# Optimization experiments

Hardware: AMD Instinct MI355X
Metric: run time of the kernel (lower is better)

## Reference

```python
import jax, jax.numpy as jnp
import numpy as np

POOL = 16  # in_downsampling == internal_downsampling == 16


def _conv1x1(x, w, b):
    # x: [B,C,H,W], w: [O,C], b: [O] -> [B,O,H,W]
    return jnp.einsum('oc,bchw->bohw', w, x) + b[None, :, None, None]


def _maxpool(x, k):
    return jax.lax.reduce_window(x, -jnp.inf, jax.lax.max,
                                 (1, 1, k, k), (1, 1, k, k), 'VALID')


def setup_inputs() -> dict:
    key = jax.random.key(0)
    ks = jax.random.split(key, 7)
    B, C, Ci, H, W = 4, 256, 128, 256, 256
    s_in = 1.0 / np.sqrt(C)
    return {
        'x':   jax.random.normal(ks[0], (B, C, H, W), jnp.float32),
        'f_w': jax.random.normal(ks[1], (Ci, C), jnp.float32) * s_in,
        'f_b': jax.random.normal(ks[2], (Ci,), jnp.float32) * 0.01,
        'g_w': jax.random.normal(ks[3], (Ci, C), jnp.float32) * s_in,
        'g_b': jax.random.normal(ks[4], (Ci,), jnp.float32) * 0.01,
        'h_w': jax.random.normal(ks[5], (C, C), jnp.float32) * s_in,
        'h_b': jax.random.normal(ks[6], (C,), jnp.float32) * 0.01,
    }


def reference(x, f_w, f_b, g_w, g_b, h_w, h_b):
    B, C, H, W = x.shape
    # pooled query / key features: [B, Ci, h1, w1] and [B, Ci, h2, w2]
    fv = _maxpool(_conv1x1(x, f_w, f_b), POOL)
    gv = _maxpool(_conv1x1(x, g_w, g_b), POOL)
    # dots[b,i,j,k,l] = sum_c fv[b,c,i,j] * gv[b,c,k,l]  (channel dot-product)
    dots = jnp.einsum('bcij,bckl->bijkl', fv, gv)
    Bd, h1, w1, h2, w2 = dots.shape
    # exp=True path: softmax over the flattened (h2, w2) key positions
    dots = jax.nn.softmax(dots.reshape(Bd, h1, w1, h2 * w2), axis=-1)
    dots = dots.reshape(Bd, h1, w1, h2, w2)
    # pooled values: [B, C, h2, w2]
    hv = _maxpool(_conv1x1(x, h_w, h_b), POOL)
    # weighted sum over key positions -> [B, C, h1, w1]
    out = jnp.einsum('bijkl,bckl->bcij', dots, hv)
    # bilinear upsample (align_corners=False == half-pixel, matches jax resize)
    up = jax.image.resize(out, (B, C, H, W), method='bilinear')
    return up + x
```

## Files before the change

### kernel.cpp

```cpp
#include <hip/hip_runtime.h>
#include <hip/hip_fp16.h>

typedef _Float16 f16;
typedef _Float16 f16x4_t __attribute__((ext_vector_type(4)));
typedef _Float16 f16x8_t __attribute__((ext_vector_type(8)));
typedef float    f32x4_t __attribute__((ext_vector_type(4)));

#define NB  4
#define NC  256
#define NH  256
#define NW  256

__global__ __launch_bounds__(256) void k_convert_w(
    const float* __restrict__ f_w, const float* __restrict__ g_w,
    const float* __restrict__ h_w, f16* __restrict__ wf)
{
    int id = blockIdx.x * 256 + threadIdx.x;
    int cout = id >> 8;
    float v;
    if (cout < 128)       v = f_w[id];
    else if (cout < 256)  v = g_w[id - 128*256];
    else                  v = h_w[id - 256*256];
    wf[id] = (f16)v;
}

__device__ __forceinline__ void bar_lds() {
    asm volatile("s_waitcnt lgkmcnt(0)" ::: "memory");
    __builtin_amdgcn_s_barrier();
}

__global__ __launch_bounds__(1024, 4) void k_pooled_conv(
    const float* __restrict__ x, const f16* __restrict__ wf,
    const float* __restrict__ f_b, const float* __restrict__ g_b,
    const float* __restrict__ h_b,
    float* __restrict__ pooled_fg,
    float* __restrict__ pooledT_h)
{
    __shared__ __align__(16) char smem[65536];

    const int t    = threadIdx.x;
    const int wave = t >> 6;
    const int lane = t & 63;
    const int l15  = lane & 15;
    const int lg   = lane >> 4;
    const bool isfg = (wave < 8);
    const int coutbase = isfg ? wave * 32 : 256 + (wave - 8) * 32;

    f16x8_t bfrag[2][8];
    #pragma unroll
    for (int n = 0; n < 2; n++) {
        const f16* wr = wf + (coutbase + n*16 + l15) * 256 + lg*8;
        #pragma unroll
        for (int k = 0; k < 8; k++)
            bfrag[n][k] = *(const f16x8_t*)(wr + k*32);
    }
    float biasv[2];
    #pragma unroll
    for (int n = 0; n < 2; n++) {
        int c = coutbase + n*16 + l15;
        biasv[n] = (c < 128) ? f_b[c] : (c < 256) ? g_b[c - 128] : h_b[c - 256];
    }

    const int dx  = t & 15;
    const int dyl = (t >> 4) & 1;
    const int c8  = (t >> 5) * 8;
    const unsigned page = (unsigned)(dyl*8 + (c8 >> 5));
    const unsigned slot = (unsigned)(dx | (((c8 >> 3) & 3) << 4));
    const unsigned woff = (page << 10) + slot * 16u;

    const int bid   = blockIdx.x;
    const int b     = bid >> 6;
    const int wbase = bid * 4;
    const float* xb = x + (size_t)b * (256u * 65536u);

    float vmax[2] = {-3.0e38f, -3.0e38f};

    auto loadst = [&](int gsd, float* r) {
        int win = wbase + (gsd >> 3);
        int s   = gsd & 7;
        int wi = (win >> 4) & 15, wj = win & 15;
        const float* src = xb + (size_t)c8 * 65536u
                         + (unsigned)((wi*16 + s*2 + dyl) * 256 + wj*16 + dx);
        #pragma unroll
        for (int cc = 0; cc < 8; cc++)
            r[cc] = src[(unsigned)cc * 65536u];
    };
    auto writest = [&](const float* r, int buf) {
        char* base = smem + buf * 32768;
        f16x8_t hv, lv;
        #pragma unroll
        for (int cc = 0; cc < 8; cc++) {
            float v = r[cc];
            f16 h = (f16)v;
            hv[cc] = h;
            lv[cc] = (f16)(v - (float)h);
        }
        *(f16x8_t*)(base + woff)         = hv;
        *(f16x8_t*)(base + 16384 + woff) = lv;
    };
    auto mfmast = [&](int buf) {
        const char* base = smem + buf * 32768 + lane * 16;
        #pragma unroll
        for (int m = 0; m < 2; m++) {
            f32x4_t acc0 = {0.f,0.f,0.f,0.f}, acc1 = {0.f,0.f,0.f,0.f};
            #pragma unroll
            for (int k = 0; k < 8; k++) {
                const char* p = base + ((m*8 + k) << 10);
                f16x8_t ah = *(const f16x8_t*)p;
                acc0 = __builtin_amdgcn_mfma_f32_16x16x32_f16(ah, bfrag[0][k], acc0, 0,0,0);
                acc1 = __builtin_amdgcn_mfma_f32_16x16x32_f16(ah, bfrag[1][k], acc1, 0,0,0);
                if (isfg) {
                    f16x8_t al = *(const f16x8_t*)(p + 16384);
                    acc0 = __builtin_amdgcn_mfma_f32_16x16x32_f16(al, bfrag[0][k], acc0, 0,0,0);
                    acc1 = __builtin_amdgcn_mfma_f32_16x16x32_f16(al, bfrag[1][k], acc1, 0,0,0);
                }
            }
            #pragma unroll
            for (int r = 0; r < 4; r++) {
                vmax[0] = fmaxf(vmax[0], acc0[r]);
                vmax[1] = fmaxf(vmax[1], acc1[r]);
            }
        }
    };
    auto finalize = [&](int win) {
        int wn = win & 255;
        #pragma unroll
        for (int n = 0; n < 2; n++) {
            float v = vmax[n];
            v = fmaxf(v, __shfl_xor(v, 16, 64));
            v = fmaxf(v, __shfl_xor(v, 32, 64));
            if (lane < 16) {
                float val = v + biasv[n];
                int c = coutbase + n*16 + lane;
                if (isfg) pooled_fg[((b*256 + c)  << 8) + wn] = val;
                else      pooledT_h[((b*256 + wn) << 8) + (c - 256)] = val;
            }
            vmax[n] = -3.0e38f;
        }
    };

    float rA[8], rB[8];
    loadst(0, rA);
    loadst(1, rB);
    writest(rA, 0);
    bar_lds();

    #pragma unroll 1
    for (int gs = 0; gs < 32; gs += 2) {
        if (gs + 2 < 32) loadst(gs + 2, rA);
        writest(rB, 1);
        mfmast(0);
        bar_lds();
        if (gs + 3 < 32) loadst(gs + 3, rB);
        if (gs + 2 < 32) writest(rA, 0);
        mfmast(1);
        if ((gs & 7) == 6) finalize(wbase + (gs >> 3));
        bar_lds();
    }
}

__global__ __launch_bounds__(256) void k_attn(
    const float* __restrict__ pooled_fg, const float* __restrict__ pooledT_h,
    float* __restrict__ attnout)
{
    __shared__ float red[4];
    __shared__ float p_lds[256];
    const int blk = blockIdx.x;
    const int b = blk >> 8;
    const int q = blk & 255;
    const int t = threadIdx.x;

    const float* fv = pooled_fg + ((b*256) << 8) + q;
    const float* gv = pooled_fg + ((b*256 + 128) << 8) + t;

    float s = 0.f;
    #pragma unroll 8
    for (int c = 0; c < 128; c++)
        s += fv[c << 8] * gv[c << 8];

    float m = s;
    #pragma unroll
    for (int o = 1; o < 64; o <<= 1) m = fmaxf(m, __shfl_xor(m, o, 64));
    if ((t & 63) == 0) red[t >> 6] = m;
    __syncthreads();
    m = fmaxf(fmaxf(red[0], red[1]), fmaxf(red[2], red[3]));
    __syncthreads();

    float p = expf(s - m);
    float sum = p;
    #pragma unroll
    for (int o = 1; o < 64; o <<= 1) sum += __shfl_xor(sum, o, 64);
    if ((t & 63) == 0) red[t >> 6] = sum;
    __syncthreads();
    sum = red[0] + red[1] + red[2] + red[3];
    p /= sum;
    p_lds[t] = p;
    __syncthreads();

    const float* hv = pooledT_h + (b << 16) + t;
    float acc = 0.f;
    #pragma unroll 8
    for (int k = 0; k < 256; k++)
        acc += p_lds[k] * hv[k << 8];
    attnout[((b*256 + t) << 8) + q] = acc;
}

__global__ __launch_bounds__(256) void k_upsample_add(
    const float* __restrict__ x, const float* __restrict__ attnout,
    float* __restrict__ out)
{
    __shared__ float L[256];
    const int blk = blockIdx.x;
    const int t = threadIdx.x;
    L[t] = attnout[(blk << 8) + t];
    __syncthreads();
    const float* xp = x   + (size_t)blk * 65536;
    float*       op = out + (size_t)blk * 65536;

    const int x4 = (t & 63) << 2;
    const int yo = t >> 6;
    float fxv[4]; int x0v[4], x1v[4];
    #pragma unroll
    for (int e = 0; e < 4; e++) {
        float sx  = (x4 + e + 0.5f) * 0.0625f - 0.5f;
        float x0f = floorf(sx);
        fxv[e] = sx - x0f;
        int ix0 = (int)x0f;
        x0v[e] = min(15, max(0, ix0));
        x1v[e] = min(15, max(0, ix0 + 1));
    }
    for (int it = 0; it < 64; it++) {
        int y = it*4 + yo;
        float sy  = (y + 0.5f) * 0.0625f - 0.5f;
        float y0f = floorf(sy);
        float fy  = sy - y0f;
        int iy0 = (int)y0f;
        int y0 = min(15, max(0, iy0));
        int y1 = min(15, max(0, iy0 + 1));
        const float* Ly0 = L + y0*16;
        const float* Ly1 = L + y1*16;
        float4 xin = *(const float4*)(xp + y*256 + x4);
        float o[4]; const float* xe = (const float*)&xin;
        #pragma unroll
        for (int e = 0; e < 4; e++) {
            float top = Ly0[x0v[e]] + fxv[e] * (Ly0[x1v[e]] - Ly0[x0v[e]]);
            float bot = Ly1[x0v[e]] + fxv[e] * (Ly1[x1v[e]] - Ly1[x0v[e]]);
            o[e] = top + fy * (bot - top) + xe[e];
        }
        float4 ov = make_float4(o[0], o[1], o[2], o[3]);
        *(float4*)(op + y*256 + x4) = ov;
    }
}

extern "C" void kernel_launch(void* const* d_in, const int* in_sizes, int n_in,
                              void* d_out, int out_size, void* d_ws, size_t ws_size,
                              hipStream_t stream)
{
    const float* x   = (const float*)d_in[0];
    const float* f_w = (const float*)d_in[1];
    const float* f_b = (const float*)d_in[2];
    const float* g_w = (const float*)d_in[3];
    const float* g_b = (const float*)d_in[4];
    const float* h_w = (const float*)d_in[5];
    const float* h_b = (const float*)d_in[6];
    float* out = (float*)d_out;

    char* ws = (char*)d_ws;
    f16*   wf        = (f16*)ws;
    float* pooled_fg = (float*)(ws + (256<<10));
    float* pooledT_h = (float*)(ws + (256<<10) + (1<<20));
    float* attnout   = (float*)(ws + (256<<10) + (2<<20));

    k_convert_w   <<<512, 256, 0, stream>>>(f_w, g_w, h_w, wf);
    k_pooled_conv <<<256, 1024, 0, stream>>>(x, wf, f_b, g_b, h_b, pooled_fg, pooledT_h);
    k_attn        <<<1024, 256, 0, stream>>>(pooled_fg, pooledT_h, attnout);
    k_upsample_add<<<1024, 256, 0, stream>>>(x, attnout, out);
}
```

Measured before the change: 293.7 us.

## Split conv stage into barrier-synchronized phases with MFMA priority boost

Restructures the pooled-conv main loop so each stage runs as eight phases. Each phase issues its LDS reads, then hits a workgroup barrier, then runs its MFMA cluster under raised wave priority via s_setprio. Global loads and LDS writes for the next stage are issued inside the first phase, so memory traffic interleaves with matrix work across waves. This adds many more barriers per stage (16 instead of 1) in a 1024-thread block, which risks extra sync overhead. The max-reduction is also split to run twice per stage.

```diff
diff --git a/kernel.cpp b/kernel.cpp
--- a/kernel.cpp
+++ b/kernel.cpp
@@ -24,11 +24,6 @@
     wf[id] = (f16)v;
 }
 
-__device__ __forceinline__ void bar_lds() {
-    asm volatile("s_waitcnt lgkmcnt(0)" ::: "memory");
-    __builtin_amdgcn_s_barrier();
-}
-
 __global__ __launch_bounds__(1024, 4) void k_pooled_conv(
     const float* __restrict__ x, const f16* __restrict__ wf,
     const float* __restrict__ f_b, const float* __restrict__ g_b,
@@ -97,30 +92,6 @@
         }
         *(f16x8_t*)(base + woff)         = hv;
         *(f16x8_t*)(base + 16384 + woff) = lv;
-    };
-    auto mfmast = [&](int buf) {
-        const char* base = smem + buf * 32768 + lane * 16;
-        #pragma unroll
-        for (int m = 0; m < 2; m++) {
-            f32x4_t acc0 = {0.f,0.f,0.f,0.f}, acc1 = {0.f,0.f,0.f,0.f};
-            #pragma unroll
-            for (int k = 0; k < 8; k++) {
-                const char* p = base + ((m*8 + k) << 10);
-                f16x8_t ah = *(const f16x8_t*)p;
-                acc0 = __builtin_amdgcn_mfma_f32_16x16x32_f16(ah, bfrag[0][k], acc0, 0,0,0);
-                acc1 = __builtin_amdgcn_mfma_f32_16x16x32_f16(ah, bfrag[1][k], acc1, 0,0,0);
-                if (isfg) {
-                    f16x8_t al = *(const f16x8_t*)(p + 16384);
-                    acc0 = __builtin_amdgcn_mfma_f32_16x16x32_f16(al, bfrag[0][k], acc0, 0,0,0);
-                    acc1 = __builtin_amdgcn_mfma_f32_16x16x32_f16(al, bfrag[1][k], acc1, 0,0,0);
-                }
-            }
-            #pragma unroll
-            for (int r = 0; r < 4; r++) {
-                vmax[0] = fmaxf(vmax[0], acc0[r]);
-                vmax[1] = fmaxf(vmax[1], acc1[r]);
-            }
-        }
     };
     auto finalize = [&](int win) {
         int wn = win & 255;
@@ -139,23 +110,65 @@
         }
     };
 
+    auto stagebody = [&](int s, int cur, float* rLoad, const float* rWrite) {
+        f32x4_t acc0 = {0.f,0.f,0.f,0.f}, acc1 = {0.f,0.f,0.f,0.f};
+        #pragma unroll
+        for (int ph = 0; ph < 8; ph++) {
+            const int m  = ph >> 2;
+            const int k0 = (ph & 3) * 2;
+            const char* rb = smem + cur * 32768 + ((m*8 + k0) << 10) + lane * 16;
+            f16x8_t ah0 = *(const f16x8_t*)rb;
+            f16x8_t ah1 = *(const f16x8_t*)(rb + 1024);
+            f16x8_t al0 = {}, al1 = {};
+            if (isfg) {
+                al0 = *(const f16x8_t*)(rb + 16384);
+                al1 = *(const f16x8_t*)(rb + 16384 + 1024);
+            }
+            if (ph == 0) {
+                if (s + 2 < 32) loadst(s + 2, rLoad);
+                if (s + 1 < 32) writest(rWrite, cur ^ 1);
+            }
+            __builtin_amdgcn_s_barrier();
+            asm volatile("s_waitcnt lgkmcnt(0)" ::: "memory");
+            __builtin_amdgcn_s_setprio(1);
+            acc0 = __builtin_amdgcn_mfma_f32_16x16x32_f16(ah0, bfrag[0][k0], acc0, 0,0,0);
+            acc1 = __builtin_amdgcn_mfma_f32_16x16x32_f16(ah0, bfrag[1][k0], acc1, 0,0,0);
+            if (isfg) {
+                acc0 = __builtin_amdgcn_mfma_f32_16x16x32_f16(al0, bfrag[0][k0], acc0, 0,0,0);
+                acc1 = __builtin_amdgcn_mfma_f32_16x16x32_f16(al0, bfrag[1][k0], acc1, 0,0,0);
+            }
+            acc0 = __builtin_amdgcn_mfma_f32_16x16x32_f16(ah1, bfrag[0][k0+1], acc0, 0,0,0);
+            acc1 = __builtin_amdgcn_mfma_f32_16x16x32_f16(ah1, bfrag[1][k0+1], acc1, 0,0,0);
+            if (isfg) {
+                acc0 = __builtin_amdgcn_mfma_f32_16x16x32_f16(al1, bfrag[0][k0+1], acc0, 0,0,0);
+                acc1 = __builtin_amdgcn_mfma_f32_16x16x32_f16(al1, bfrag[1][k0+1], acc1, 0,0,0);
+            }
+            __builtin_amdgcn_s_setprio(0);
+            __builtin_amdgcn_s_barrier();
+            if (ph == 3 || ph == 7) {
+                #pragma unroll
+                for (int r = 0; r < 4; r++) {
+                    vmax[0] = fmaxf(vmax[0], acc0[r]);
+                    vmax[1] = fmaxf(vmax[1], acc1[r]);
+                }
+                acc0 = (f32x4_t){0.f,0.f,0.f,0.f};
+                acc1 = (f32x4_t){0.f,0.f,0.f,0.f};
+            }
+        }
+    };
+
     float rA[8], rB[8];
     loadst(0, rA);
     loadst(1, rB);
     writest(rA, 0);
-    bar_lds();
+    asm volatile("s_waitcnt lgkmcnt(0)" ::: "memory");
+    __builtin_amdgcn_s_barrier();
 
     #pragma unroll 1
-    for (int gs = 0; gs < 32; gs += 2) {
-        if (gs + 2 < 32) loadst(gs + 2, rA);
-        writest(rB, 1);
-        mfmast(0);
-        bar_lds();
-        if (gs + 3 < 32) loadst(gs + 3, rB);
-        if (gs + 2 < 32) writest(rA, 0);
-        mfmast(1);
-        if ((gs & 7) == 6) finalize(wbase + (gs >> 3));
-        bar_lds();
+    for (int s2 = 0; s2 < 32; s2 += 2) {
+        stagebody(s2,     0, rA, rB);
+        stagebody(s2 + 1, 1, rB, rA);
+        if ((s2 & 7) == 6) finalize(wbase + (s2 >> 3));
     }
 }
 
```

Measured after the change: 390.6 us. 33.0% more time.
